# Optimization experiments

Hardware: AMD Instinct MI355X
Metric: run time of the kernel (lower is better)

Reference implementation:

```python
import jax, jax.numpy as jnp
import numpy as np

OBS_DIM, ACT_DIM, K, H1, H2, B = 128, 32, 16, 1024, 1024, 4096


def _init_linear(key, shape, fan_in):
    # torch nn.Linear-style uniform init U(-1/sqrt(fan_in), 1/sqrt(fan_in))
    bound = 1.0 / np.sqrt(fan_in)
    return jax.random.uniform(key, shape, jnp.float32, -bound, bound)


def setup_inputs() -> dict:
    key = jax.random.key(0)
    ks = jax.random.split(key, 9)
    in1 = OBS_DIM + ACT_DIM
    return {
        "obs": jax.random.normal(ks[0], (B, OBS_DIM), jnp.float32),
        "actions": jax.random.normal(ks[1], (B, ACT_DIM), jnp.float32),
        "comp_weights": jax.random.uniform(ks[2], (B, K), jnp.float32),
        "W1": _init_linear(ks[3], (K, in1, H1), in1),
        "b1": _init_linear(ks[4], (K, H1), in1),
        "W2": _init_linear(ks[5], (K, H1, H2), H1),
        "b2": _init_linear(ks[6], (K, H2), H1),
        "Wo": _init_linear(ks[7], (H2, 1), H2),
        "bo": _init_linear(ks[8], (1,), H2),
    }


def _comp_fc(x, cw, W, b, activate=True):
    # per-parameter-set projection: [B, K, out]
    y = jnp.einsum("bi,kio->bko", x, W) + b[None, :, :]
    # soft composition over K param sets: [B, out]
    y = jnp.einsum("bko,bk->bo", y, cw)
    return jax.nn.relu(y) if activate else y


def reference(obs, actions, comp_weights, W1, b1, W2, b2, Wo, bo):
    x = jnp.concatenate([obs, actions], axis=-1)  # [B, obs+act]
    x = _comp_fc(x, comp_weights, W1, b1)
    x = _comp_fc(x, comp_weights, W2, b2)
    return x @ Wo + bo  # [B, 1]
```

## Files before the change

### kernel.cpp

```cpp
#include <hip/hip_runtime.h>

typedef unsigned short u16;
typedef unsigned int   u32;
typedef __bf16 bf16x8 __attribute__((ext_vector_type(8)));
typedef float  f32x4  __attribute__((ext_vector_type(4)));

#define BSZ   4096
#define NK    16
#define IN1   160
#define H1D   1024
#define H2D   1024
#define K1MAIN 2560
#define K1P    2624
#define K2P    16384

__device__ __forceinline__ u16 f2bf(float f) {
    __bf16 h = (__bf16)f;
    return __builtin_bit_cast(u16, h);
}
__device__ __forceinline__ u32 pack2bf(float lo, float hi) {
    return (u32)f2bf(lo) | ((u32)f2bf(hi) << 16);
}

__device__ __forceinline__ void gload16(const void* g, void* l) {
    __builtin_amdgcn_global_load_lds(
        (const __attribute__((address_space(1))) unsigned int*)g,
        (__attribute__((address_space(3))) unsigned int*)l, 16, 0, 0);
}

__global__ void transpose_conv_kernel(const float* __restrict__ W,
                                      const float* __restrict__ bias,
                                      u16* __restrict__ outw,
                                      int Kdim, int KP)
{
    __shared__ float lt[64][65];
    const int k0 = blockIdx.x * 64, n0 = blockIdx.y * 64;
    const int c = threadIdx.x & 63, r0 = threadIdx.x >> 6;
#pragma unroll
    for (int rr = 0; rr < 16; ++rr) {
        const int r = r0 + rr * 4;
        const int kap = k0 + r;
        float v = 0.0f;
        if (kap < Kdim)            v = W[(size_t)kap * 1024 + n0 + c];
        else if (kap < Kdim + NK)  v = bias[(size_t)(kap - Kdim) * 1024 + n0 + c];
        lt[r][c] = v;
    }
    __syncthreads();
#pragma unroll
    for (int it = 0; it < 2; ++it) {
        const int q = it * 256 + threadIdx.x;
        const int nl = q >> 3, kc = q & 7;
        uint4 o;
        o.x = pack2bf(lt[kc * 8 + 0][nl], lt[kc * 8 + 1][nl]);
        o.y = pack2bf(lt[kc * 8 + 2][nl], lt[kc * 8 + 3][nl]);
        o.z = pack2bf(lt[kc * 8 + 4][nl], lt[kc * 8 + 5][nl]);
        o.w = pack2bf(lt[kc * 8 + 6][nl], lt[kc * 8 + 7][nl]);
        *reinterpret_cast<uint4*>(&outw[(size_t)(n0 + nl) * KP + k0 + kc * 8]) = o;
    }
}

__global__ __launch_bounds__(256, 2)
void gemm1_kernel(const float* __restrict__ obs,
                  const float* __restrict__ act,
                  const float* __restrict__ cw,
                  const u16* __restrict__ Bt,
                  u16* __restrict__ H1)
{
    __shared__ u16 lA[2][128 * 64];
    __shared__ u16 lB[2][64 * 64];

    const int tid = threadIdx.x;
    const int wv = tid >> 6, lane = tid & 63;
    const int l15 = lane & 15, lg = lane >> 4;
    const int bid = blockIdx.x;
    const int ntile = bid & 15, mtile = bid >> 4;
    const int brow = mtile * 128, bcol = ntile * 64;
    const int wr = (wv >> 1) * 64, wc = (wv & 1) * 32;

    f32x4 acc[4][2];
#pragma unroll
    for (int i = 0; i < 4; ++i)
#pragma unroll
        for (int j = 0; j < 2; ++j) acc[i][j] = (f32x4){0.f, 0.f, 0.f, 0.f};

    auto stageA = [&](int kt, int buf) {
#pragma unroll
        for (int it = 0; it < 4; ++it) {
            const int c = it * 256 + tid;
            const int row = c >> 3, kb = (c & 7) << 4;
            const int lkb = kb ^ ((row & 7) << 4);
            const int b_ = brow + row;
            uint4 dat;
            const int kap = kt * 64 + (lkb >> 1);
            if (kap < K1MAIN) {
                const int k = kap / IN1;
                const int i = kap - k * IN1;
                const float s = cw[b_ * NK + k];
                const float* src = (i < 128) ? (obs + (size_t)b_ * 128 + i)
                                             : (act + (size_t)b_ * 32 + (i - 128));
                float4 f0 = *reinterpret_cast<const float4*>(src);
                float4 f1 = *reinterpret_cast<const float4*>(src + 4);
                dat.x = pack2bf(f0.x * s, f0.y * s);
                dat.y = pack2bf(f0.z * s, f0.w * s);
                dat.z = pack2bf(f1.x * s, f1.y * s);
                dat.w = pack2bf(f1.z * s, f1.w * s);
            } else {
                const int base = kap - K1MAIN;
                u16 v[8];
#pragma unroll
                for (int e = 0; e < 8; ++e) {
                    const int kk2 = base + e;
                    v[e] = (kk2 < NK) ? f2bf(cw[b_ * NK + kk2]) : (u16)0;
                }
                dat.x = (u32)v[0] | ((u32)v[1] << 16);
                dat.y = (u32)v[2] | ((u32)v[3] << 16);
                dat.z = (u32)v[4] | ((u32)v[5] << 16);
                dat.w = (u32)v[6] | ((u32)v[7] << 16);
            }
            *reinterpret_cast<uint4*>(&lA[buf][row * 64 + (kb >> 1)]) = dat;
        }
    };
    auto stageB = [&](int kt, int buf) {
#pragma unroll
        for (int it = 0; it < 2; ++it) {
            const int c = it * 256 + tid;
            const int row = c >> 3, kb = (c & 7) << 4;
            const int kbS = kb ^ ((row & 7) << 4);
            gload16(Bt + (size_t)(bcol + row) * K1P + kt * 64 + (kbS >> 1),
                    &lB[buf][(it * 256 + (wv << 6)) * 8]);
        }
    };

    const int ksteps = K1P / 64;
    stageA(0, 0);
    stageB(0, 0);
    __syncthreads();
    int cur = 0;
    for (int kt = 0; kt < ksteps; ++kt) {
        if (kt + 1 < ksteps) { stageB(kt + 1, cur ^ 1); stageA(kt + 1, cur ^ 1); }
#pragma unroll
        for (int kk = 0; kk < 2; ++kk) {
            bf16x8 af[4];
            bf16x8 bfr[2];
            const int kbyte = (kk << 6) | (lg << 4);
#pragma unroll
            for (int mi = 0; mi < 4; ++mi) {
                const int r = wr + mi * 16 + l15;
                const int sl = kbyte ^ ((r & 7) << 4);
                af[mi] = *reinterpret_cast<const bf16x8*>(&lA[cur][r * 64 + (sl >> 1)]);
            }
#pragma unroll
            for (int ni = 0; ni < 2; ++ni) {
                const int r = wc + ni * 16 + l15;
                const int sl = kbyte ^ ((r & 7) << 4);
                bfr[ni] = *reinterpret_cast<const bf16x8*>(&lB[cur][r * 64 + (sl >> 1)]);
            }
#pragma unroll
            for (int mi = 0; mi < 4; ++mi)
#pragma unroll
                for (int ni = 0; ni < 2; ++ni)
                    acc[mi][ni] = __builtin_amdgcn_mfma_f32_16x16x32_bf16(
                        af[mi], bfr[ni], acc[mi][ni], 0, 0, 0);
        }
        __syncthreads();
        cur ^= 1;
    }
#pragma unroll
    for (int mi = 0; mi < 4; ++mi)
#pragma unroll
        for (int ni = 0; ni < 2; ++ni)
#pragma unroll
            for (int r = 0; r < 4; ++r) {
                float v = fmaxf(acc[mi][ni][r], 0.0f);
                const int gm = brow + wr + mi * 16 + lg * 4 + r;
                const int gn = bcol + wc + ni * 16 + l15;
                H1[(size_t)gm * 1024 + gn] = f2bf(v);
            }
}

__global__ __launch_bounds__(256, 2)
void gemm2_kernel(const u16* __restrict__ h1,
                  const float* __restrict__ cw,
                  const float* __restrict__ b2,
                  const u16* __restrict__ Bt,
                  float* __restrict__ H2)
{
    __shared__ u16 lA[2][128 * 64];
    __shared__ u16 lB[2][64 * 64];

    const int tid = threadIdx.x;
    const int wv = tid >> 6, lane = tid & 63;
    const int l15 = lane & 15, lg = lane >> 4;
    const int bid = blockIdx.x;
    const int ntile = bid & 15, mtile = bid >> 4;
    const int brow = mtile * 128, bcol = ntile * 64;
    const int wr = (wv >> 1) * 64, wc = (wv & 1) * 32;

    f32x4 part[4][2], master[4][2];
#pragma unroll
    for (int i = 0; i < 4; ++i)
#pragma unroll
        for (int j = 0; j < 2; ++j) {
            part[i][j] = (f32x4){0.f, 0.f, 0.f, 0.f};
            master[i][j] = (f32x4){0.f, 0.f, 0.f, 0.f};
        }

    auto stageA = [&](int kt, int buf) {
        const int j0 = (kt & 15) * 64;
#pragma unroll
        for (int it = 0; it < 4; ++it) {
            const int c = it * 256 + tid;
            const int row = c >> 3, kb = (c & 7) << 4;
            const int kbS = kb ^ ((row & 7) << 4);
            gload16(h1 + (size_t)(brow + row) * 1024 + j0 + (kbS >> 1),
                    &lA[buf][(it * 256 + (wv << 6)) * 8]);
        }
    };
    auto stageB = [&](int kt, int buf) {
#pragma unroll
        for (int it = 0; it < 2; ++it) {
            const int c = it * 256 + tid;
            const int row = c >> 3, kb = (c & 7) << 4;
            const int kbS = kb ^ ((row & 7) << 4);
            gload16(Bt + (size_t)(bcol + row) * K2P + kt * 64 + (kbS >> 1),
                    &lB[buf][(it * 256 + (wv << 6)) * 8]);
        }
    };

    float cwv[4][4];
    float b2v[2];

    const int ksteps = K2P / 64;
    stageB(0, 0);
    stageA(0, 0);
    __syncthreads();
    int cur = 0;
    for (int kt = 0; kt < ksteps; ++kt) {
        if (kt + 1 < ksteps) { stageB(kt + 1, cur ^ 1); stageA(kt + 1, cur ^ 1); }
        if ((kt & 15) == 0) {
            const int kg = kt >> 4;
#pragma unroll
            for (int mi = 0; mi < 4; ++mi)
#pragma unroll
                for (int r = 0; r < 4; ++r)
                    cwv[mi][r] = cw[(brow + wr + mi * 16 + lg * 4 + r) * NK + kg];
#pragma unroll
            for (int ni = 0; ni < 2; ++ni)
                b2v[ni] = b2[kg * 1024 + bcol + wc + ni * 16 + l15];
        }
#pragma unroll
        for (int kk = 0; kk < 2; ++kk) {
            bf16x8 af[4];
            bf16x8 bfr[2];
            const int kbyte = (kk << 6) | (lg << 4);
#pragma unroll
            for (int mi = 0; mi < 4; ++mi) {
                const int r = wr + mi * 16 + l15;
                const int sl = kbyte ^ ((r & 7) << 4);
                af[mi] = *reinterpret_cast<const bf16x8*>(&lA[cur][r * 64 + (sl >> 1)]);
            }
#pragma unroll
            for (int ni = 0; ni < 2; ++ni) {
                const int r = wc + ni * 16 + l15;
                const int sl = kbyte ^ ((r & 7) << 4);
                bfr[ni] = *reinterpret_cast<const bf16x8*>(&lB[cur][r * 64 + (sl >> 1)]);
            }
#pragma unroll
            for (int mi = 0; mi < 4; ++mi)
#pragma unroll
                for (int ni = 0; ni < 2; ++ni)
                    part[mi][ni] = __builtin_amdgcn_mfma_f32_16x16x32_bf16(
                        af[mi], bfr[ni], part[mi][ni], 0, 0, 0);
        }
        if ((kt & 15) == 15) {
#pragma unroll
            for (int mi = 0; mi < 4; ++mi)
#pragma unroll
                for (int ni = 0; ni < 2; ++ni)
#pragma unroll
                    for (int r = 0; r < 4; ++r) {
                        master[mi][ni][r] += cwv[mi][r] * (part[mi][ni][r] + b2v[ni]);
                        part[mi][ni][r] = 0.0f;
                    }
        }
        __syncthreads();
        cur ^= 1;
    }
#pragma unroll
    for (int mi = 0; mi < 4; ++mi)
#pragma unroll
        for (int ni = 0; ni < 2; ++ni)
#pragma unroll
            for (int r = 0; r < 4; ++r) {
                float v = fmaxf(master[mi][ni][r], 0.0f);
                const int gm = brow + wr + mi * 16 + lg * 4 + r;
                const int gn = bcol + wc + ni * 16 + l15;
                H2[(size_t)gm * 1024 + gn] = v;
            }
}

__global__ void gemv_out_kernel(const float* __restrict__ h2,
                                const float* __restrict__ Wo,
                                const float* __restrict__ bo,
                                float* __restrict__ out)
{
    const int wv = threadIdx.x >> 6, lane = threadIdx.x & 63;
    const int row = blockIdx.x * 4 + wv;
    const float* hr = h2 + (size_t)row * 1024;
    float s = 0.0f;
#pragma unroll
    for (int i = 0; i < 4; ++i) {
        float4 h = *reinterpret_cast<const float4*>(hr + lane * 4 + i * 256);
        float4 w = *reinterpret_cast<const float4*>(Wo + lane * 4 + i * 256);
        s += h.x * w.x + h.y * w.y + h.z * w.z + h.w * w.w;
    }
#pragma unroll
    for (int off = 32; off; off >>= 1) s += __shfl_xor(s, off, 64);
    if (lane == 0) out[row] = s + bo[0];
}

extern "C" void kernel_launch(void* const* d_in, const int* in_sizes, int n_in,
                              void* d_out, int out_size, void* d_ws, size_t ws_size,
                              hipStream_t stream)
{
    const float* obs = (const float*)d_in[0];
    const float* act = (const float*)d_in[1];
    const float* cw  = (const float*)d_in[2];
    const float* W1  = (const float*)d_in[3];
    const float* b1  = (const float*)d_in[4];
    const float* W2  = (const float*)d_in[5];
    const float* b2  = (const float*)d_in[6];
    const float* Wo  = (const float*)d_in[7];
    const float* bo  = (const float*)d_in[8];

    char* ws = (char*)d_ws;
    u16* W1T = (u16*)ws;
    u16* W2T = W1T + (size_t)H1D * K1P;
    u16* H1  = W2T + (size_t)H2D * K2P;
    float* H2 = (float*)(H1 + (size_t)BSZ * H1D);

    transpose_conv_kernel<<<dim3(K1P / 64, 16), 256, 0, stream>>>(W1, b1, W1T, K1MAIN, K1P);
    transpose_conv_kernel<<<dim3(K2P / 64, 16), 256, 0, stream>>>(W2, b2, W2T, K2P, K2P);

    gemm1_kernel<<<512, 256, 0, stream>>>(obs, act, cw, W1T, H1);
    gemm2_kernel<<<512, 256, 0, stream>>>(H1, cw, b2, W2T, H2);

    gemv_out_kernel<<<BSZ / 4, 256, 0, stream>>>(H2, Wo, bo, (float*)d_out);
}
```

Before: 425.0 us.

## Enlarge gemm2 tile to 128x128 and split K across two halves

```diff
diff --git a/kernel.cpp b/kernel.cpp
--- a/kernel.cpp
+++ b/kernel.cpp
@@ -183,24 +183,28 @@
                   const float* __restrict__ cw,
                   const float* __restrict__ b2,
                   const u16* __restrict__ Bt,
-                  float* __restrict__ H2)
+                  float* __restrict__ H2a,
+                  float* __restrict__ H2b)
 {
     __shared__ u16 lA[2][128 * 64];
-    __shared__ u16 lB[2][64 * 64];
+    __shared__ u16 lB[2][128 * 64];
 
     const int tid = threadIdx.x;
     const int wv = tid >> 6, lane = tid & 63;
     const int l15 = lane & 15, lg = lane >> 4;
     const int bid = blockIdx.x;
-    const int ntile = bid & 15, mtile = bid >> 4;
-    const int brow = mtile * 128, bcol = ntile * 64;
-    const int wr = (wv >> 1) * 64, wc = (wv & 1) * 32;
-
-    f32x4 part[4][2], master[4][2];
+    const int kc = bid >> 8;
+    const int r8 = bid & 255;
+    const int ntile = r8 & 7, mtile = r8 >> 3;
+    const int brow = mtile * 128, bcol = ntile * 128;
+    const int wr = (wv >> 1) * 64, wc = (wv & 1) * 64;
+    const size_t kbase = (size_t)kc * 8192;
+
+    f32x4 part[4][4], master[4][4];
 #pragma unroll
     for (int i = 0; i < 4; ++i)
 #pragma unroll
-        for (int j = 0; j < 2; ++j) {
+        for (int j = 0; j < 4; ++j) {
             part[i][j] = (f32x4){0.f, 0.f, 0.f, 0.f};
             master[i][j] = (f32x4){0.f, 0.f, 0.f, 0.f};
         }
@@ -218,19 +222,19 @@
     };
     auto stageB = [&](int kt, int buf) {
 #pragma unroll
-        for (int it = 0; it < 2; ++it) {
+        for (int it = 0; it < 4; ++it) {
             const int c = it * 256 + tid;
             const int row = c >> 3, kb = (c & 7) << 4;
             const int kbS = kb ^ ((row & 7) << 4);
-            gload16(Bt + (size_t)(bcol + row) * K2P + kt * 64 + (kbS >> 1),
+            gload16(Bt + (size_t)(bcol + row) * K2P + kbase + kt * 64 + (kbS >> 1),
                     &lB[buf][(it * 256 + (wv << 6)) * 8]);
         }
     };
 
     float cwv[4][4];
-    float b2v[2];
-
-    const int ksteps = K2P / 64;
+    float b2v[4];
+
+    const int ksteps = 128;
     stageB(0, 0);
     stageA(0, 0);
     __syncthreads();
@@ -238,20 +242,20 @@
     for (int kt = 0; kt < ksteps; ++kt) {
         if (kt + 1 < ksteps) { stageB(kt + 1, cur ^ 1); stageA(kt + 1, cur ^ 1); }
         if ((kt & 15) == 0) {
-            const int kg = kt >> 4;
+            const int kg = kc * 8 + (kt >> 4);
 #pragma unroll
             for (int mi = 0; mi < 4; ++mi)
 #pragma unroll
                 for (int r = 0; r < 4; ++r)
                     cwv[mi][r] = cw[(brow + wr + mi * 16 + lg * 4 + r) * NK + kg];
 #pragma unroll
-            for (int ni = 0; ni < 2; ++ni)
+            for (int ni = 0; ni < 4; ++ni)
                 b2v[ni] = b2[kg * 1024 + bcol + wc + ni * 16 + l15];
         }
 #pragma unroll
         for (int kk = 0; kk < 2; ++kk) {
             bf16x8 af[4];
-            bf16x8 bfr[2];
+            bf16x8 bfr[4];
             const int kbyte = (kk << 6) | (lg << 4);
 #pragma unroll
             for (int mi = 0; mi < 4; ++mi) {
@@ -260,7 +264,7 @@
                 af[mi] = *reinterpret_cast<const bf16x8*>(&lA[cur][r * 64 + (sl >> 1)]);
             }
 #pragma unroll
-            for (int ni = 0; ni < 2; ++ni) {
+            for (int ni = 0; ni < 4; ++ni) {
                 const int r = wc + ni * 16 + l15;
                 const int sl = kbyte ^ ((r & 7) << 4);
                 bfr[ni] = *reinterpret_cast<const bf16x8*>(&lB[cur][r * 64 + (sl >> 1)]);
@@ -268,7 +272,7 @@
 #pragma unroll
             for (int mi = 0; mi < 4; ++mi)
 #pragma unroll
-                for (int ni = 0; ni < 2; ++ni)
+                for (int ni = 0; ni < 4; ++ni)
                     part[mi][ni] = __builtin_amdgcn_mfma_f32_16x16x32_bf16(
                         af[mi], bfr[ni], part[mi][ni], 0, 0, 0);
         }
@@ -276,7 +280,7 @@
 #pragma unroll
             for (int mi = 0; mi < 4; ++mi)
 #pragma unroll
-                for (int ni = 0; ni < 2; ++ni)
+                for (int ni = 0; ni < 4; ++ni)
 #pragma unroll
                     for (int r = 0; r < 4; ++r) {
                         master[mi][ni][r] += cwv[mi][r] * (part[mi][ni][r] + b2v[ni]);
@@ -286,33 +290,37 @@
         __syncthreads();
         cur ^= 1;
     }
+    float* __restrict__ dst = kc ? H2b : H2a;
 #pragma unroll
     for (int mi = 0; mi < 4; ++mi)
 #pragma unroll
-        for (int ni = 0; ni < 2; ++ni)
+        for (int ni = 0; ni < 4; ++ni)
 #pragma unroll
             for (int r = 0; r < 4; ++r) {
-                float v = fmaxf(master[mi][ni][r], 0.0f);
                 const int gm = brow + wr + mi * 16 + lg * 4 + r;
                 const int gn = bcol + wc + ni * 16 + l15;
-                H2[(size_t)gm * 1024 + gn] = v;
-            }
-}
-
-__global__ void gemv_out_kernel(const float* __restrict__ h2,
+                dst[(size_t)gm * 1024 + gn] = master[mi][ni][r];
+            }
+}
+
+__global__ void gemv_out_kernel(const float* __restrict__ h2a,
+                                const float* __restrict__ h2b,
                                 const float* __restrict__ Wo,
                                 const float* __restrict__ bo,
                                 float* __restrict__ out)
 {
     const int wv = threadIdx.x >> 6, lane = threadIdx.x & 63;
     const int row = blockIdx.x * 4 + wv;
-    const float* hr = h2 + (size_t)row * 1024;
+    const float* ha = h2a + (size_t)row * 1024;
+    const float* hb = h2b + (size_t)row * 1024;
     float s = 0.0f;
 #pragma unroll
     for (int i = 0; i < 4; ++i) {
-        float4 h = *reinterpret_cast<const float4*>(hr + lane * 4 + i * 256);
+        float4 a = *reinterpret_cast<const float4*>(ha + lane * 4 + i * 256);
+        float4 b = *reinterpret_cast<const float4*>(hb + lane * 4 + i * 256);
         float4 w = *reinterpret_cast<const float4*>(Wo + lane * 4 + i * 256);
-        s += h.x * w.x + h.y * w.y + h.z * w.z + h.w * w.w;
+        s += fmaxf(a.x + b.x, 0.f) * w.x + fmaxf(a.y + b.y, 0.f) * w.y
+           + fmaxf(a.z + b.z, 0.f) * w.z + fmaxf(a.w + b.w, 0.f) * w.w;
     }
 #pragma unroll
     for (int off = 32; off; off >>= 1) s += __shfl_xor(s, off, 64);
@@ -334,16 +342,17 @@
     const float* bo  = (const float*)d_in[8];
 
     char* ws = (char*)d_ws;
-    u16* W1T = (u16*)ws;
-    u16* W2T = W1T + (size_t)H1D * K1P;
-    u16* H1  = W2T + (size_t)H2D * K2P;
-    float* H2 = (float*)(H1 + (size_t)BSZ * H1D);
+    u16* W1T  = (u16*)ws;
+    u16* W2T  = W1T + (size_t)H1D * K1P;
+    u16* H1   = W2T + (size_t)H2D * K2P;
+    float* H2a = (float*)(H1 + (size_t)BSZ * H1D);
+    float* H2b = H2a + (size_t)BSZ * H2D;
 
     transpose_conv_kernel<<<dim3(K1P / 64, 16), 256, 0, stream>>>(W1, b1, W1T, K1MAIN, K1P);
     transpose_conv_kernel<<<dim3(K2P / 64, 16), 256, 0, stream>>>(W2, b2, W2T, K2P, K2P);
 
     gemm1_kernel<<<512, 256, 0, stream>>>(obs, act, cw, W1T, H1);
-    gemm2_kernel<<<512, 256, 0, stream>>>(H1, cw, b2, W2T, H2);
-
-    gemv_out_kernel<<<BSZ / 4, 256, 0, stream>>>(H2, Wo, bo, (float*)d_out);
-}
+    gemm2_kernel<<<512, 256, 0, stream>>>(H1, cw, b2, W2T, H2a, H2b);
+
+    gemv_out_kernel<<<BSZ / 4, 256, 0, stream>>>(H2a, H2b, Wo, bo, (float*)d_out);
+}
```

Measured after the change: 357.0 us. 16.0% less time.
